# Kernel optimization log

Measured on AMD Instinct MI355X. Metric: run time of the kernel, lower is better.

Reference implementation:

```python
import jax, jax.numpy as jnp
import numpy as np

B, D, H, W = 1, 16, 16, 16
C, NH = 528, 8
HD = C // NH      # 66
K = 32            # retrieved memories per token


def setup_inputs() -> dict:
    key = jax.random.key(0)
    ks = jax.random.split(key, 4)
    x = jax.random.normal(ks[0], (B, D, H, W, C), jnp.float32)
    # simulated knn_memory.search output: (B, heads, N, K, 2[k/v], head_dim)
    knn_kv = jax.random.normal(ks[1], (B, NH, D * H * W, K, 2, HD), jnp.float32)
    w_qkv = jax.random.normal(ks[2], (3 * C, C), jnp.float32) * 0.02
    b_qkv = jnp.zeros((3 * C,), jnp.float32)
    w_proj = jax.random.normal(ks[3], (C, C), jnp.float32) * 0.02
    b_proj = jnp.zeros((C,), jnp.float32)
    return {"x": x, "knn_kv": knn_kv, "w_qkv": w_qkv, "b_qkv": b_qkv,
            "w_proj": w_proj, "b_proj": b_proj, "num_heads": NH}


def _l2norm(t):
    # F.normalize(t, dim=-1): t / max(||t||_2, eps)
    n = jnp.linalg.norm(t, axis=-1, keepdims=True)
    return t / jnp.maximum(n, 1e-12)


def _forward(x, knn_kv, w_qkv, b_qkv, w_proj, b_proj, num_heads):
    Bb, Dd, Hh, Ww, Cc = x.shape
    N = Dd * Hh * Ww
    hd = Cc // num_heads
    scaling = hd ** -0.5
    qkv = x.reshape(Bb * N, Cc) @ w_qkv.T + b_qkv
    qkv = qkv.reshape(Bb, N, 3, num_heads, hd).transpose(2, 0, 3, 1, 4)  # (3,B,h,N,hd)
    q, k, v = qkv[0], qkv[1], qkv[2]
    q = _l2norm(q)
    k = _l2norm(k)
    knn_k = knn_kv[..., 0, :]   # (B,h,N,K,hd)
    knn_v = knn_kv[..., 1, :]
    k_comb = jnp.concatenate([knn_k, k[..., None, :]], axis=-2)  # (B,h,N,K+1,hd)
    v_comb = jnp.concatenate([knn_v, v[..., None, :]], axis=-2)
    attn = jnp.einsum('bhnd,bhnkd->bhnk', q, k_comb) * scaling
    attn = jax.nn.softmax(attn, axis=-1)  # stable softmax
    out = jnp.einsum('bhnk,bhnkd->bhnd', attn, v_comb)  # (B,h,N,hd)
    out = out.transpose(0, 2, 1, 3).reshape(Bb * N, num_heads * hd)
    out = out @ w_proj.T + b_proj
    return out.reshape(Bb, Dd, Hh, Ww, Cc)


def reference(x, knn_kv, w_qkv, b_qkv, w_proj, b_proj, num_heads):
    return _forward(x, knn_kv, w_qkv, b_qkv, w_proj, b_proj, num_heads)
```

## Files before the change

### kernel.cpp

```cpp
#include <hip/hip_runtime.h>
#include <hip/hip_bf16.h>
#include <math.h>

#define N_POS 4096
#define C_DIM 528
#define NHEAD 8
#define HDIM  66
#define KNN   32
#define CQKV  1584
#define KP    544
#define NP1   1664
#define NP2   640

typedef __attribute__((ext_vector_type(8))) short short8;
typedef __attribute__((ext_vector_type(4))) float f32x4;
typedef __hip_bfloat16 bf16;

typedef const __attribute__((address_space(1))) void* gas1;
typedef __attribute__((address_space(3))) void* las3;

__global__ __launch_bounds__(256) void convpad3_kernel(
    const float* __restrict__ x, const float* __restrict__ wq,
    const float* __restrict__ wp,
    bf16* __restrict__ xb, bf16* __restrict__ wqb, bf16* __restrict__ wpb)
{
    int b = blockIdx.x;
    const float* src; bf16* dst; int Nr;
    if (b < N_POS)            { src = x;  dst = xb;  Nr = N_POS; }
    else if (b < N_POS + NP1) { b -= N_POS; src = wq; dst = wqb; Nr = CQKV; }
    else                      { b -= N_POS + NP1; src = wp; dst = wpb; Nr = C_DIM; }
    for (int c = threadIdx.x; c < KP; c += 256) {
        float v = (b < Nr && c < C_DIM) ? src[(size_t)b * C_DIM + c] : 0.0f;
        dst[(size_t)b * KP + c] = __float2bfloat16(v);
    }
}

__global__ __launch_bounds__(256) void gemm_mfma_kernel(
    const bf16* __restrict__ A, const bf16* __restrict__ B,
    const float* __restrict__ bias, float* __restrict__ C,
    int Nreal, int ldc)
{
    __shared__ bf16 As[2][128 * 32];
    __shared__ bf16 Bs[2][128 * 32];

    const int tid  = threadIdx.x;
    const int lane = tid & 63;
    const int wid  = tid >> 6;
    const int bm = blockIdx.y * 128;
    const int bn = blockIdx.x * 128;

    const int r_lo = (wid << 5) + (lane >> 2);
    const int r_hi = r_lo + 16;
    const int csw  = ((lane & 3) ^ ((r_lo >> 1) & 3)) << 3;

    const bf16* Agl = A + (size_t)(bm + r_lo) * KP + csw;
    const bf16* Agh = A + (size_t)(bm + r_hi) * KP + csw;
    const bf16* Bgl = B + (size_t)(bn + r_lo) * KP + csw;
    const bf16* Bgh = B + (size_t)(bn + r_hi) * KP + csw;

    bf16* as0 = &As[0][0] + (wid << 5) * 32;
    bf16* bs0 = &Bs[0][0] + (wid << 5) * 32;
    const int BUF = 128 * 32;

    const int wm = (wid >> 1) * 64;
    const int wn = (wid & 1) * 64;
    const int arow = wm + (lane & 15);
    const int brow = wn + (lane & 15);
    const int seg  = lane >> 4;
    const int aoff = (seg ^ ((arow >> 1) & 3)) << 3;
    const int boff = (seg ^ ((brow >> 1) & 3)) << 3;

    f32x4 acc[4][4];
    #pragma unroll
    for (int i = 0; i < 4; ++i)
        #pragma unroll
        for (int j = 0; j < 4; ++j)
            acc[i][j] = (f32x4){0.f, 0.f, 0.f, 0.f};

    __builtin_amdgcn_global_load_lds((gas1)(Agl), (las3)(as0),            16, 0, 0);
    __builtin_amdgcn_global_load_lds((gas1)(Agh), (las3)(as0 + 16 * 32),  16, 0, 0);
    __builtin_amdgcn_global_load_lds((gas1)(Bgl), (las3)(bs0),            16, 0, 0);
    __builtin_amdgcn_global_load_lds((gas1)(Bgh), (las3)(bs0 + 16 * 32),  16, 0, 0);
    __syncthreads();

    int cur = 0;
    for (int k0 = 0; k0 < KP; k0 += 32) {
        if (k0 + 32 < KP) {
            const int nb = cur ^ 1;
            __builtin_amdgcn_global_load_lds((gas1)(Agl + k0 + 32), (las3)(as0 + nb * BUF),           16, 0, 0);
            __builtin_amdgcn_global_load_lds((gas1)(Agh + k0 + 32), (las3)(as0 + nb * BUF + 16 * 32), 16, 0, 0);
            __builtin_amdgcn_global_load_lds((gas1)(Bgl + k0 + 32), (las3)(bs0 + nb * BUF),           16, 0, 0);
            __builtin_amdgcn_global_load_lds((gas1)(Bgh + k0 + 32), (las3)(bs0 + nb * BUF + 16 * 32), 16, 0, 0);
        }

        const bf16* ab = &As[cur][0];
        const bf16* bb = &Bs[cur][0];
        short8 af[4], bfr[4];
        #pragma unroll
        for (int f = 0; f < 4; ++f)
            af[f] = *(const short8*)&ab[(arow + f * 16) * 32 + aoff];
        #pragma unroll
        for (int f = 0; f < 4; ++f)
            bfr[f] = *(const short8*)&bb[(brow + f * 16) * 32 + boff];

        #pragma unroll
        for (int i = 0; i < 4; ++i)
            #pragma unroll
            for (int j = 0; j < 4; ++j)
                acc[i][j] = __builtin_amdgcn_mfma_f32_16x16x32_bf16(
                    af[i], bfr[j], acc[i][j], 0, 0, 0);

        __syncthreads();
        cur ^= 1;
    }

    #pragma unroll
    for (int i = 0; i < 4; ++i) {
        const int row = bm + wm + i * 16 + (lane >> 4) * 4;
        #pragma unroll
        for (int j = 0; j < 4; ++j) {
            const int col = bn + wn + j * 16 + (lane & 15);
            if (col < Nreal) {
                const float bv = bias[col];
                #pragma unroll
                for (int r = 0; r < 4; ++r)
                    C[(size_t)(row + r) * ldc + col] = acc[i][j][r] + bv;
            }
        }
    }
}

__global__ __launch_bounds__(256) void attn_kernel(
    const float* __restrict__ qkv, const float* __restrict__ knn,
    bf16* __restrict__ out)
{
    const float scaling = 0.12309149097933272f;

    int bid = blockIdx.x;
    int h = bid >> 12;
    int n = bid & 4095;
    int tid = threadIdx.x;

    __shared__ float s_knn[KNN * 2 * HDIM];
    __shared__ float s_q[HDIM], s_k[HDIM], s_v[HDIM];
    __shared__ float s_dot[KNN + 1];
    __shared__ float s_scale[2];

    {
        const float4* src = (const float4*)(knn + ((size_t)bid) * (KNN * 2 * HDIM));
        float4* dst = (float4*)s_knn;
        for (int i = tid; i < KNN * 2 * HDIM / 4; i += 256) dst[i] = src[i];
    }
    const float* qp = qkv + (size_t)n * CQKV + h * HDIM;
    if (tid < HDIM) {
        s_q[tid] = qp[tid];
        s_k[tid] = qp[C_DIM + tid];
        s_v[tid] = qp[2 * C_DIM + tid];
    }
    __syncthreads();

    if (tid < 64) {
        float aq = s_q[tid] * s_q[tid];
        float ak = s_k[tid] * s_k[tid];
        if (tid < 2) {
            aq += s_q[64 + tid] * s_q[64 + tid];
            ak += s_k[64 + tid] * s_k[64 + tid];
        }
        #pragma unroll
        for (int off = 32; off; off >>= 1) {
            aq += __shfl_xor(aq, off);
            ak += __shfl_xor(ak, off);
        }
        if (tid == 0) {
            s_scale[0] = 1.0f / fmaxf(sqrtf(aq), 1e-12f);
            s_scale[1] = 1.0f / fmaxf(sqrtf(ak), 1e-12f);
        }
    }
    __syncthreads();
    if (tid < HDIM) {
        s_q[tid] *= s_scale[0];
        s_k[tid] *= s_scale[1];
    }
    __syncthreads();

    {
        int g = tid >> 3, l8 = tid & 7;
        float p = 0.f;
        for (int d = l8; d < HDIM; d += 8) p += s_q[d] * s_knn[g * (2 * HDIM) + d];
        p += __shfl_xor(p, 1);
        p += __shfl_xor(p, 2);
        p += __shfl_xor(p, 4);
        if (l8 == 0) s_dot[g] = p * scaling;
    }
    if (tid < 8) {
        float p = 0.f;
        for (int d = tid; d < HDIM; d += 8) p += s_q[d] * s_k[d];
        p += __shfl_xor(p, 1);
        p += __shfl_xor(p, 2);
        p += __shfl_xor(p, 4);
        if (tid == 0) s_dot[KNN] = p * scaling;
    }
    __syncthreads();

    if (tid < 64) {
        float x = (tid < 33) ? s_dot[tid] : -3.4e38f;
        float m = x;
        #pragma unroll
        for (int off = 32; off; off >>= 1) m = fmaxf(m, __shfl_xor(m, off));
        float e = (tid < 33) ? expf(x - m) : 0.f;
        float s = e;
        #pragma unroll
        for (int off = 32; off; off >>= 1) s += __shfl_xor(s, off);
        if (tid < 33) s_dot[tid] = e / s;
    }
    __syncthreads();

    if (tid < HDIM) {
        float acc = s_dot[KNN] * s_v[tid];
        #pragma unroll 8
        for (int k = 0; k < KNN; ++k)
            acc += s_dot[k] * s_knn[k * (2 * HDIM) + HDIM + tid];
        out[(size_t)n * KP + h * HDIM + tid] = __float2bfloat16(acc);
    }
    if (h == 0 && tid < KP - C_DIM) {
        out[(size_t)n * KP + C_DIM + tid] = __float2bfloat16(0.0f);
    }
}

extern "C" void kernel_launch(void* const* d_in, const int* in_sizes, int n_in,
                              void* d_out, int out_size, void* d_ws, size_t ws_size,
                              hipStream_t stream)
{
    const float* x      = (const float*)d_in[0];
    const float* knn_kv = (const float*)d_in[1];
    const float* w_qkv  = (const float*)d_in[2];
    const float* b_qkv  = (const float*)d_in[3];
    const float* w_proj = (const float*)d_in[4];
    const float* b_proj = (const float*)d_in[5];
    float* out = (float*)d_out;

    char* ws = (char*)d_ws;
    float* qkv = (float*)ws;
    bf16*  xb  = (bf16*)(ws + 25952256);
    bf16*  wqb = (bf16*)(ws + 25952256 + 4456448);
    bf16*  wpb = (bf16*)(ws + 25952256 + 4456448 + 1810432);
    bf16*  ab  = (bf16*)(ws + 25952256 + 4456448 + 1810432 + 696320);

    convpad3_kernel<<<N_POS + NP1 + NP2, 256, 0, stream>>>(x, w_qkv, w_proj, xb, wqb, wpb);

    gemm_mfma_kernel<<<dim3(NP1 / 128, N_POS / 128), 256, 0, stream>>>(
        xb, wqb, b_qkv, qkv, CQKV, CQKV);

    attn_kernel<<<dim3(NHEAD * N_POS), 256, 0, stream>>>(qkv, knn_kv, ab);

    gemm_mfma_kernel<<<dim3(NP2 / 128, N_POS / 128), 256, 0, stream>>>(
        ab, wpb, b_proj, out, C_DIM, C_DIM);
}
```

Measured before the change: 188.2 us.

## Use wave-per-token attention with register shuffles and smaller GEMM tiles

```diff
diff --git a/kernel.cpp b/kernel.cpp
--- a/kernel.cpp
+++ b/kernel.cpp
@@ -40,73 +40,66 @@
     const float* __restrict__ bias, float* __restrict__ C,
     int Nreal, int ldc)
 {
-    __shared__ bf16 As[2][128 * 32];
-    __shared__ bf16 Bs[2][128 * 32];
+    __shared__ bf16 As[2][64 * 32];
+    __shared__ bf16 Bs[2][64 * 32];
 
     const int tid  = threadIdx.x;
     const int lane = tid & 63;
     const int wid  = tid >> 6;
-    const int bm = blockIdx.y * 128;
-    const int bn = blockIdx.x * 128;
-
-    const int r_lo = (wid << 5) + (lane >> 2);
-    const int r_hi = r_lo + 16;
-    const int csw  = ((lane & 3) ^ ((r_lo >> 1) & 3)) << 3;
-
-    const bf16* Agl = A + (size_t)(bm + r_lo) * KP + csw;
-    const bf16* Agh = A + (size_t)(bm + r_hi) * KP + csw;
-    const bf16* Bgl = B + (size_t)(bn + r_lo) * KP + csw;
-    const bf16* Bgh = B + (size_t)(bn + r_hi) * KP + csw;
-
-    bf16* as0 = &As[0][0] + (wid << 5) * 32;
-    bf16* bs0 = &Bs[0][0] + (wid << 5) * 32;
-    const int BUF = 128 * 32;
-
-    const int wm = (wid >> 1) * 64;
-    const int wn = (wid & 1) * 64;
+    const int bm = blockIdx.y * 64;
+    const int bn = blockIdx.x * 64;
+
+    const int r   = (wid << 4) + (lane >> 2);
+    const int csw = ((lane & 3) ^ ((r >> 1) & 3)) << 3;
+
+    const bf16* Ag = A + (size_t)(bm + r) * KP + csw;
+    const bf16* Bg = B + (size_t)(bn + r) * KP + csw;
+
+    bf16* as0 = &As[0][0] + (wid << 4) * 32;
+    bf16* bs0 = &Bs[0][0] + (wid << 4) * 32;
+    const int BUF = 64 * 32;
+
+    const int wm = (wid >> 1) * 32;
+    const int wn = (wid & 1) * 32;
     const int arow = wm + (lane & 15);
     const int brow = wn + (lane & 15);
     const int seg  = lane >> 4;
     const int aoff = (seg ^ ((arow >> 1) & 3)) << 3;
     const int boff = (seg ^ ((brow >> 1) & 3)) << 3;
 
-    f32x4 acc[4][4];
-    #pragma unroll
-    for (int i = 0; i < 4; ++i)
-        #pragma unroll
-        for (int j = 0; j < 4; ++j)
+    f32x4 acc[2][2];
+    #pragma unroll
+    for (int i = 0; i < 2; ++i)
+        #pragma unroll
+        for (int j = 0; j < 2; ++j)
             acc[i][j] = (f32x4){0.f, 0.f, 0.f, 0.f};
 
-    __builtin_amdgcn_global_load_lds((gas1)(Agl), (las3)(as0),            16, 0, 0);
-    __builtin_amdgcn_global_load_lds((gas1)(Agh), (las3)(as0 + 16 * 32),  16, 0, 0);
-    __builtin_amdgcn_global_load_lds((gas1)(Bgl), (las3)(bs0),            16, 0, 0);
-    __builtin_amdgcn_global_load_lds((gas1)(Bgh), (las3)(bs0 + 16 * 32),  16, 0, 0);
+    __builtin_amdgcn_global_load_lds((gas1)(Ag), (las3)(as0), 16, 0, 0);
+    __builtin_amdgcn_global_load_lds((gas1)(Bg), (las3)(bs0), 16, 0, 0);
     __syncthreads();
 
     int cur = 0;
     for (int k0 = 0; k0 < KP; k0 += 32) {
         if (k0 + 32 < KP) {
             const int nb = cur ^ 1;
-            __builtin_amdgcn_global_load_lds((gas1)(Agl + k0 + 32), (las3)(as0 + nb * BUF),           16, 0, 0);
-            __builtin_amdgcn_global_load_lds((gas1)(Agh + k0 + 32), (las3)(as0 + nb * BUF + 16 * 32), 16, 0, 0);
-            __builtin_amdgcn_global_load_lds((gas1)(Bgl + k0 + 32), (las3)(bs0 + nb * BUF),           16, 0, 0);
-            __builtin_amdgcn_global_load_lds((gas1)(Bgh + k0 + 32), (las3)(bs0 + nb * BUF + 16 * 32), 16, 0, 0);
+            __builtin_amdgcn_global_load_lds((gas1)(Ag + k0 + 32), (las3)(as0 + nb * BUF), 16, 0, 0);
+            __builtin_amdgcn_global_load_lds((gas1)(Bg + k0 + 32), (las3)(bs0 + nb * BUF), 16, 0, 0);
         }
 
         const bf16* ab = &As[cur][0];
         const bf16* bb = &Bs[cur][0];
-        short8 af[4], bfr[4];
-        #pragma unroll
-        for (int f = 0; f < 4; ++f)
+        short8 af[2], bfr[2];
+        #pragma unroll
+        for (int f = 0; f < 2; ++f)
             af[f] = *(const short8*)&ab[(arow + f * 16) * 32 + aoff];
         #pragma unroll
-        for (int f = 0; f < 4; ++f)
+        for (int f = 0; f < 2; ++f)
             bfr[f] = *(const short8*)&bb[(brow + f * 16) * 32 + boff];
 
         #pragma unroll
-        for (int i = 0; i < 4; ++i)
+        for (int i = 0; i < 2; ++i)
             #pragma unroll
-            for (int j = 0; j < 4; ++j)
+            for (int j = 0; j < 2; ++j)
                 acc[i][j] = __builtin_amdgcn_mfma_f32_16x16x32_bf16(
                     af[i], bfr[j], acc[i][j], 0, 0, 0);
 
@@ -115,16 +108,16 @@
     }
 
     #pragma unroll
-    for (int i = 0; i < 4; ++i) {
+    for (int i = 0; i < 2; ++i) {
         const int row = bm + wm + i * 16 + (lane >> 4) * 4;
         #pragma unroll
-        for (int j = 0; j < 4; ++j) {
+        for (int j = 0; j < 2; ++j) {
             const int col = bn + wn + j * 16 + (lane & 15);
             if (col < Nreal) {
                 const float bv = bias[col];
                 #pragma unroll
-                for (int r = 0; r < 4; ++r)
-                    C[(size_t)(row + r) * ldc + col] = acc[i][j][r] + bv;
+                for (int rr = 0; rr < 4; ++rr)
+                    C[(size_t)(row + rr) * ldc + col] = acc[i][j][rr] + bv;
             }
         }
     }
@@ -136,95 +129,82 @@
 {
     const float scaling = 0.12309149097933272f;
 
-    int bid = blockIdx.x;
-    int h = bid >> 12;
-    int n = bid & 4095;
-    int tid = threadIdx.x;
-
-    __shared__ float s_knn[KNN * 2 * HDIM];
-    __shared__ float s_q[HDIM], s_k[HDIM], s_v[HDIM];
-    __shared__ float s_dot[KNN + 1];
-    __shared__ float s_scale[2];
-
+    const int gw   = (blockIdx.x << 2) + (threadIdx.x >> 6);
+    const int lane = threadIdx.x & 63;
+    const int h = gw >> 12;
+    const int n = gw & 4095;
+    const bool act = lane < 33;
+
+    const float* qp = qkv + (size_t)n * CQKV + h * HDIM;
+    float2 q2 = {0.f, 0.f}, k2 = {0.f, 0.f}, v2 = {0.f, 0.f};
+    if (act) {
+        q2 = *(const float2*)(qp + 2 * lane);
+        k2 = *(const float2*)(qp + C_DIM + 2 * lane);
+        v2 = *(const float2*)(qp + 2 * C_DIM + 2 * lane);
+    }
+
+    float sq = q2.x * q2.x + q2.y * q2.y;
+    float sk = k2.x * k2.x + k2.y * k2.y;
+    #pragma unroll
+    for (int off = 32; off; off >>= 1) {
+        sq += __shfl_xor(sq, off);
+        sk += __shfl_xor(sk, off);
+    }
+    const float iq = 1.0f / fmaxf(sqrtf(sq), 1e-12f);
+    const float ik = 1.0f / fmaxf(sqrtf(sk), 1e-12f);
+    q2.x *= iq; q2.y *= iq;
+    k2.x *= ik; k2.y *= ik;
+
+    const float* kb = knn + (size_t)gw * (KNN * 2 * HDIM);
+    float p = -3.4e38f;
+    float2 vr[KNN + 1];
+    #pragma unroll
+    for (int j = 0; j < KNN; ++j) {
+        float2 kj = {0.f, 0.f}, vj = {0.f, 0.f};
+        if (act) {
+            kj = *(const float2*)(kb + j * 132 + 2 * lane);
+            vj = *(const float2*)(kb + j * 132 + HDIM + 2 * lane);
+        }
+        vr[j] = vj;
+        float d = q2.x * kj.x + q2.y * kj.y;
+        #pragma unroll
+        for (int off = 32; off; off >>= 1) d += __shfl_xor(d, off);
+        if (lane == j) p = d * scaling;
+    }
+    vr[KNN] = v2;
     {
-        const float4* src = (const float4*)(knn + ((size_t)bid) * (KNN * 2 * HDIM));
-        float4* dst = (float4*)s_knn;
-        for (int i = tid; i < KNN * 2 * HDIM / 4; i += 256) dst[i] = src[i];
-    }
-    const float* qp = qkv + (size_t)n * CQKV + h * HDIM;
-    if (tid < HDIM) {
-        s_q[tid] = qp[tid];
-        s_k[tid] = qp[C_DIM + tid];
-        s_v[tid] = qp[2 * C_DIM + tid];
-    }
-    __syncthreads();
-
-    if (tid < 64) {
-        float aq = s_q[tid] * s_q[tid];
-        float ak = s_k[tid] * s_k[tid];
-        if (tid < 2) {
-            aq += s_q[64 + tid] * s_q[64 + tid];
-            ak += s_k[64 + tid] * s_k[64 + tid];
-        }
-        #pragma unroll
-        for (int off = 32; off; off >>= 1) {
-            aq += __shfl_xor(aq, off);
-            ak += __shfl_xor(ak, off);
-        }
-        if (tid == 0) {
-            s_scale[0] = 1.0f / fmaxf(sqrtf(aq), 1e-12f);
-            s_scale[1] = 1.0f / fmaxf(sqrtf(ak), 1e-12f);
-        }
-    }
-    __syncthreads();
-    if (tid < HDIM) {
-        s_q[tid] *= s_scale[0];
-        s_k[tid] *= s_scale[1];
-    }
-    __syncthreads();
-
-    {
-        int g = tid >> 3, l8 = tid & 7;
-        float p = 0.f;
-        for (int d = l8; d < HDIM; d += 8) p += s_q[d] * s_knn[g * (2 * HDIM) + d];
-        p += __shfl_xor(p, 1);
-        p += __shfl_xor(p, 2);
-        p += __shfl_xor(p, 4);
-        if (l8 == 0) s_dot[g] = p * scaling;
-    }
-    if (tid < 8) {
-        float p = 0.f;
-        for (int d = tid; d < HDIM; d += 8) p += s_q[d] * s_k[d];
-        p += __shfl_xor(p, 1);
-        p += __shfl_xor(p, 2);
-        p += __shfl_xor(p, 4);
-        if (tid == 0) s_dot[KNN] = p * scaling;
-    }
-    __syncthreads();
-
-    if (tid < 64) {
-        float x = (tid < 33) ? s_dot[tid] : -3.4e38f;
-        float m = x;
-        #pragma unroll
-        for (int off = 32; off; off >>= 1) m = fmaxf(m, __shfl_xor(m, off));
-        float e = (tid < 33) ? expf(x - m) : 0.f;
-        float s = e;
-        #pragma unroll
-        for (int off = 32; off; off >>= 1) s += __shfl_xor(s, off);
-        if (tid < 33) s_dot[tid] = e / s;
-    }
-    __syncthreads();
-
-    if (tid < HDIM) {
-        float acc = s_dot[KNN] * s_v[tid];
-        #pragma unroll 8
-        for (int k = 0; k < KNN; ++k)
-            acc += s_dot[k] * s_knn[k * (2 * HDIM) + HDIM + tid];
-        out[(size_t)n * KP + h * HDIM + tid] = __float2bfloat16(acc);
-    }
-    if (h == 0 && tid < KP - C_DIM) {
-        out[(size_t)n * KP + C_DIM + tid] = __float2bfloat16(0.0f);
-    }
+        float d = q2.x * k2.x + q2.y * k2.y;
+        #pragma unroll
+        for (int off = 32; off; off >>= 1) d += __shfl_xor(d, off);
+        if (lane == KNN) p = d * scaling;
+    }
+
+    float m = p;
+    #pragma unroll
+    for (int off = 32; off; off >>= 1) m = fmaxf(m, __shfl_xor(m, off));
+    float e = expf(p - m);
+    float s = e;
+    #pragma unroll
+    for (int off = 32; off; off >>= 1) s += __shfl_xor(s, off);
+    const float pr = e / s;
+
+    float2 acc = {0.f, 0.f};
+    #pragma unroll
+    for (int j = 0; j <= KNN; ++j) {
+        const float pj = __shfl(pr, j);
+        acc.x += pj * vr[j].x;
+        acc.y += pj * vr[j].y;
+    }
+
+    if (act) {
+        bf16* op = out + (size_t)n * KP + h * HDIM + 2 * lane;
+        __hip_bfloat162 o2;
+        o2.x = __float2bfloat16(acc.x);
+        o2.y = __float2bfloat16(acc.y);
+        *(__hip_bfloat162*)op = o2;
+    }
+    if (h == 0 && lane < KP - C_DIM)
+        out[(size_t)n * KP + C_DIM + lane] = __float2bfloat16(0.0f);
 }
 
 extern "C" void kernel_launch(void* const* d_in, const int* in_sizes, int n_in,
@@ -248,11 +228,11 @@
 
     convpad3_kernel<<<N_POS + NP1 + NP2, 256, 0, stream>>>(x, w_qkv, w_proj, xb, wqb, wpb);
 
-    gemm_mfma_kernel<<<dim3(NP1 / 128, N_POS / 128), 256, 0, stream>>>(
+    gemm_mfma_kernel<<<dim3(NP1 / 64, N_POS / 64), 256, 0, stream>>>(
         xb, wqb, b_qkv, qkv, CQKV, CQKV);
 
-    attn_kernel<<<dim3(NHEAD * N_POS), 256, 0, stream>>>(qkv, knn_kv, ab);
-
-    gemm_mfma_kernel<<<dim3(NP2 / 128, N_POS / 128), 256, 0, stream>>>(
+    attn_kernel<<<dim3(NHEAD * N_POS / 4), 256, 0, stream>>>(qkv, knn_kv, ab);
+
+    gemm_mfma_kernel<<<dim3(NP2 / 64, N_POS / 64), 256, 0, stream>>>(
         ab, wpb, b_proj, out, C_DIM, C_DIM);
 }
```

New measurement: 309.5 us. 1.64x slower.
